# Performance work log

Measured on AMD Instinct MI355X. Metric: run time of the kernel, lower is better.

## Reference

```python
import jax, jax.numpy as jnp
import numpy as np
from jax import lax

T_MAX, BATCH, CLASSES, L_MAX = 512, 32, 1296, 64
NINF = -jnp.inf


def _align_one(logsm, label, C, R):
    """Monotonic max-probability forced alignment for one sample.
    logsm: [T, V] log-probs, label: [L] int, C=x_len (valid frames), R=label_len.
    Returns per-frame pseudo target [T] (0-padded past C)."""
    T, V = logsm.shape
    L = label.shape[0]
    rows = jnp.arange(L)
    cols = jnp.arange(T)
    # pb[i, j] = logsm[j, label[i]], restricted to the monotonic band i <= j <= C-R+i
    pb = logsm[:, label].T  # [L, T]
    band = (cols[None, :] >= rows[:, None]) & (cols[None, :] <= C - R + rows[:, None]) & (rows[:, None] < R)
    pb = jnp.where(band, pb, NINF)

    # Forward DP over time columns: dp[i,j] = max(dp[i-1,j-1], dp[i,j-1]) + pb[i,j]
    # (strict > for the diagonal move, exactly as the original numpy code).
    dp0 = jnp.where(rows == 0, pb[:, 0], NINF)

    def step(dp, pb_col):
        shifted = jnp.concatenate([jnp.full((1,), NINF, dp.dtype), dp[:-1]])
        choice = shifted > dp  # True -> came from (i-1, j-1)
        dp_new = jnp.where(choice, shifted, dp) + pb_col
        return dp_new, choice

    _, choices = lax.scan(step, dp0, pb.T[1:])  # [T-1, L] bool
    choices = jnp.concatenate([jnp.zeros((1, L), bool), choices], axis=0)  # [T, L]

    # Backtrack from (R-1, C-1); columns j >= C emit padding 0.
    def bstep(row, jc):
        j, ch = jc
        active = j < C
        tgt = jnp.where(active, label[row], 0)
        row_new = jnp.where(active, row - ch[row].astype(row.dtype), row)
        return row_new, tgt

    row0 = (R - 1).astype(jnp.int32)
    _, targets = lax.scan(bstep, row0, (jnp.arange(T), choices), reverse=True)
    return targets  # [T]


def _make_targets(logsm, label, x_len, label_len):
    # logsm: [T, B, V] -> targets [T, B]
    return jax.vmap(_align_one, in_axes=(1, 0, 0, 0))(logsm, label, x_len, label_len).T


def setup_inputs() -> dict:
    key = jax.random.key(0)
    k0, k1, k2, k3, k4 = jax.random.split(key, 5)
    pred = jax.random.normal(k0, (T_MAX, BATCH, CLASSES), jnp.float32)
    seq_pred = jax.random.normal(k1, (T_MAX, BATCH, CLASSES), jnp.float32)
    label = jax.random.randint(k2, (BATCH, L_MAX), 0, CLASSES)
    x_len = jax.random.randint(k3, (BATCH,), T_MAX // 2, T_MAX + 1)  # >= L_MAX so band is valid
    label_len = jax.random.randint(k4, (BATCH,), 8, L_MAX + 1)
    return {"pred": pred, "seq_pred": seq_pred, "label": label, "x_len": x_len, "label_len": label_len}


def reference(pred, seq_pred, label, x_len, label_len):
    T, B, V = pred.shape
    logsm_seq = jax.nn.log_softmax(seq_pred, axis=-1)
    target = _make_targets(logsm_seq, label, x_len, label_len)  # [T, B] int
    probs = jnp.exp(logsm_seq)  # softmax(seq_pred)
    conf = jnp.take_along_axis(probs, target[..., None], axis=2)[..., 0]  # [T, B]
    smooth = (1.0 - conf) / (V - 1)
    onehot = jax.nn.one_hot(target, V, dtype=pred.dtype)  # [T, B, V]
    true_dist = jnp.where(onehot > 0, conf[..., None], smooth[..., None])
    mask = (jnp.arange(T)[:, None] < x_len[None, :]).astype(pred.dtype)  # [T, B]
    ce = jnp.sum(-true_dist * jax.nn.log_softmax(pred, axis=-1), axis=-1) * mask
    return jnp.mean(ce)
```

## Files before the change

kernel.cpp:

```cpp
#include <hip/hip_runtime.h>

#define T_MAX 512
#define BATCH 32
#define CLASSES 1296
#define L_MAX 64
#define NROWS (T_MAX * BATCH)
#define NV4 (CLASSES / 4)
#define NINF (-INFINITY)

__device__ __forceinline__ float wave_sum64(float v) {
    v += __int_as_float(__builtin_amdgcn_update_dpp(0, __float_as_int(v), 0x111, 0xF, 0xF, true));
    v += __int_as_float(__builtin_amdgcn_update_dpp(0, __float_as_int(v), 0x112, 0xF, 0xF, true));
    v += __int_as_float(__builtin_amdgcn_update_dpp(0, __float_as_int(v), 0x114, 0xF, 0xF, true));
    v += __int_as_float(__builtin_amdgcn_update_dpp(0, __float_as_int(v), 0x118, 0xF, 0xF, true));
    v += __int_as_float(__builtin_amdgcn_update_dpp(0, __float_as_int(v), 0x142, 0xF, 0xF, true));
    v += __int_as_float(__builtin_amdgcn_update_dpp(0, __float_as_int(v), 0x143, 0xF, 0xF, true));
    return v;
}

__global__ __launch_bounds__(256) void rowstats_kernel(
    const float* __restrict__ pred, const float* __restrict__ seqp,
    const int* __restrict__ label,
    float* __restrict__ lse_pred, float* __restrict__ sum_pred,
    float* __restrict__ lse_seq, float* __restrict__ pb, int* __restrict__ counter)
{
    int wid = blockIdx.x * 4 + (threadIdx.x >> 6);
    int lane = threadIdx.x & 63;
    if (wid == 0 && lane == 0) *counter = 0;
    bool isSeq = wid >= NROWS;
    int r = isSeq ? wid - NROWS : wid;
    const float* x = (isSeq ? seqp : pred) + (size_t)r * CLASSES;
    const float4* x4 = (const float4*)x;

    float4 q0 = x4[lane];
    float4 q1 = x4[lane + 64];
    float4 q2 = x4[lane + 128];
    float4 q3 = x4[lane + 192];
    float4 q4 = x4[lane + 256];
    float4 qt = make_float4(0.f, 0.f, 0.f, 0.f);
    if (lane < 4) qt = x4[320 + lane];
    int lab = 0;
    if (isSeq) lab = label[((r & 31) << 6) + lane];

    float s  = __expf(q0.x) + __expf(q0.y) + __expf(q0.z) + __expf(q0.w)
             + __expf(q1.x) + __expf(q1.y) + __expf(q1.z) + __expf(q1.w)
             + __expf(q2.x) + __expf(q2.y) + __expf(q2.z) + __expf(q2.w)
             + __expf(q3.x) + __expf(q3.y) + __expf(q3.z) + __expf(q3.w)
             + __expf(q4.x) + __expf(q4.y) + __expf(q4.z) + __expf(q4.w);
    float sx = (q0.x + q0.y + q0.z + q0.w) + (q1.x + q1.y + q1.z + q1.w)
             + (q2.x + q2.y + q2.z + q2.w) + (q3.x + q3.y + q3.z + q3.w)
             + (q4.x + q4.y + q4.z + q4.w);
    if (lane < 4) {
        s  += __expf(qt.x) + __expf(qt.y) + __expf(qt.z) + __expf(qt.w);
        sx += qt.x + qt.y + qt.z + qt.w;
    }
    s  = wave_sum64(s);
    sx = wave_sum64(sx);

    if (isSeq) {
        int b = r & 31, t = r >> 5;
        pb[(((size_t)(b << 9) + t) << 6) + lane] = x[lab];
        if (lane == 63) lse_seq[r] = __logf(s);
    } else if (lane == 63) {
        lse_pred[r] = __logf(s);
        sum_pred[r] = sx;
    }
}

__global__ __launch_bounds__(128) void align_kernel(
    const float* __restrict__ pb, const int* __restrict__ x_len,
    const int* __restrict__ label_len, int* __restrict__ tg)
{
    int b = blockIdx.x;
    int tid = threadIdx.x, w = tid >> 6, lane = tid & 63;
    int C = x_len[b], R = label_len[b];
    int limit = C - R;
    __shared__ float buf[2][4096];
    __shared__ unsigned long long ch[T_MAX];
    __shared__ int rows_s[T_MAX];
    const float* pbb = pb + ((size_t)b << 15);
    int P = (C + 63) >> 6;

    if (w == 1) {
        const float4* s4 = (const float4*)pbb;
        float4* d4 = (float4*)buf[0];
        #pragma unroll
        for (int k = 0; k < 16; ++k) d4[(k << 6) + lane] = s4[(k << 6) + lane];
    }
    __syncthreads();

    float dp = NINF;
    const int ninf_i = 0xFF800000;

    for (int p = 0; p < P; ++p) {
        if (w == 1) {
            int ldp = p + 1; if (ldp > 7) ldp = 7;
            const float4* s4 = (const float4*)(pbb + (ldp << 12));
            float4* d4 = (float4*)buf[(p + 1) & 1];
            #pragma unroll
            for (int k = 0; k < 16; ++k) d4[(k << 6) + lane] = s4[(k << 6) + lane];
        } else {
            const float* bc = buf[p & 1];
            int base = p << 6;
            unsigned long long m_local = 0ULL;
            #pragma unroll
            for (int g = 0; g < 4; ++g) {
                float v[16];
                #pragma unroll
                for (int u = 0; u < 16; ++u) v[u] = bc[((g << 4) + u) * 64 + lane];
                #pragma unroll
                for (int u = 0; u < 16; ++u) {
                    int kk = (g << 4) + u;
                    int j = base + kk;
                    if (kk == 0 && g == 0 && p == 0) {
                        dp = (lane == 0) ? v[0] : NINF;
                    } else {
                        bool inband = (lane <= j) && (lane >= j - limit) && (lane < R);
                        float val = inband ? v[u] : NINF;
                        int dpb = __float_as_int(dp);
                        int t1 = __builtin_amdgcn_update_dpp(ninf_i, dpb, 0x111, 0xF, 0xF, false);
                        int t2 = __builtin_amdgcn_update_dpp(ninf_i, dpb, 0x142, 0xF, 0xF, false);
                        float shifted = __int_as_float(((lane & 15) == 0) ? t2 : t1);
                        bool c = shifted > dp;
                        unsigned long long msk = __ballot(c);
                        dp = (c ? shifted : dp) + val;
                        m_local = (lane == kk) ? msk : m_local;
                    }
                }
            }
            ch[base + lane] = m_local;
        }
        __syncthreads();
    }

    if (tid == 0) {
        int row = R - 1;
        int j2 = C - 1;
        while (j2 >= 0) {
            int bs = j2 & ~7;
            unsigned long long m[8];
            #pragma unroll
            for (int k = 0; k < 8; ++k) m[k] = ch[bs + k];
            for (int k = j2 - bs; k >= 0; --k) {
                rows_s[bs + k] = row;
                row -= (int)((m[k] >> row) & 1ULL);
            }
            j2 = bs - 1;
        }
    }
    __syncthreads();
    for (int j = tid; j < T_MAX; j += 128)
        tg[(b << 9) + j] = (j < C) ? rows_s[j] : -1;
}

__global__ __launch_bounds__(256) void ce_kernel(
    const float* __restrict__ pred, const int* __restrict__ label,
    const int* __restrict__ x_len,
    const float* __restrict__ lse_pred, const float* __restrict__ sum_pred,
    const float* __restrict__ lse_seq, const float* __restrict__ pb,
    const int* __restrict__ tg, float* __restrict__ partials,
    int* __restrict__ counter, float* __restrict__ out)
{
    int e = blockIdx.x * 256 + threadIdx.x;
    int t = e >> 5, b = e & 31;
    float ce = 0.f;
    if (t < x_len[b]) {
        int row = tg[(b << 9) + t];
        int tgt = label[(b << 6) + row];
        float lp = lse_pred[e];
        float S = sum_pred[e] - (float)CLASSES * lp;
        float lsp_t = pred[(size_t)e * CLASSES + tgt] - lp;
        float conf = __expf(pb[(((size_t)(b << 9) + t) << 6) + row] - lse_seq[e]);
        float smooth = (1.f - conf) * (1.f / (float)(CLASSES - 1));
        ce = -((conf - smooth) * lsp_t + smooth * S);
    }
    ce = wave_sum64(ce);
    __shared__ float sm[4];
    __shared__ int amLast;
    if ((threadIdx.x & 63) == 63) sm[threadIdx.x >> 6] = ce;
    __syncthreads();
    if (threadIdx.x == 0) {
        float p = sm[0] + sm[1] + sm[2] + sm[3];
        __hip_atomic_store(&partials[blockIdx.x], p, __ATOMIC_RELEASE, __HIP_MEMORY_SCOPE_AGENT);
        amLast = (__hip_atomic_fetch_add(counter, 1, __ATOMIC_ACQ_REL, __HIP_MEMORY_SCOPE_AGENT) == 63);
    }
    __syncthreads();
    if (amLast && threadIdx.x < 64) {
        float v = __hip_atomic_load(&partials[threadIdx.x], __ATOMIC_ACQUIRE, __HIP_MEMORY_SCOPE_AGENT);
        for (int o = 32; o; o >>= 1) v += __shfl_down(v, o, 64);
        if (threadIdx.x == 0) out[0] = v * (1.0f / (float)NROWS);
    }
}

extern "C" void kernel_launch(void* const* d_in, const int* in_sizes, int n_in,
                              void* d_out, int out_size, void* d_ws, size_t ws_size,
                              hipStream_t stream) {
    const float* pred      = (const float*)d_in[0];
    const float* seq_pred  = (const float*)d_in[1];
    const int*   label     = (const int*)d_in[2];
    const int*   x_len     = (const int*)d_in[3];
    const int*   label_len = (const int*)d_in[4];
    float* out = (float*)d_out;

    float* w = (float*)d_ws;
    float* lse_pred = w;
    float* sum_pred = w + NROWS;
    float* lse_seq  = w + 2 * NROWS;
    float* pb       = w + 3 * NROWS;
    int*   tg       = (int*)(w + 3 * NROWS + (size_t)BATCH * T_MAX * 64);
    float* partials = (float*)(tg + NROWS);
    int*   counter  = (int*)(partials + 64);

    rowstats_kernel<<<(2 * NROWS) / 4, 256, 0, stream>>>(pred, seq_pred, label,
                                                         lse_pred, sum_pred, lse_seq, pb, counter);
    align_kernel<<<BATCH, 128, 0, stream>>>(pb, x_len, label_len, tg);
    ce_kernel<<<64, 256, 0, stream>>>(pred, label, x_len,
                                      lse_pred, sum_pred, lse_seq, pb, tg,
                                      partials, counter, out);
}
```

Measured before the change: 243.7 us.

## Restructure alignment DP with transposed choice bits and jump backtrack

The row-stats kernel now has each wave handle both the pred and seq_pred row for the same index, halving the grid and sharing the label load. The alignment DP pre-masks rows beyond the label length during the prefetch copy and skips the band test for blocks that lie entirely inside the band. Choice bits are stored per lane as row-major words, replacing the ballot. The serial backtrack now jumps to the highest set bit per row using clz instead of stepping frame by frame, and the rows are filled in parallel. The aim is to shorten the serial DP and backtrack latency, which depends on the exact tie and boundary semantics staying unchanged.

```diff
diff --git a/kernel.cpp b/kernel.cpp
--- a/kernel.cpp
+++ b/kernel.cpp
@@ -24,46 +24,51 @@
     float* __restrict__ lse_pred, float* __restrict__ sum_pred,
     float* __restrict__ lse_seq, float* __restrict__ pb, int* __restrict__ counter)
 {
-    int wid = blockIdx.x * 4 + (threadIdx.x >> 6);
+    int r = blockIdx.x * 4 + (threadIdx.x >> 6);
     int lane = threadIdx.x & 63;
-    if (wid == 0 && lane == 0) *counter = 0;
-    bool isSeq = wid >= NROWS;
-    int r = isSeq ? wid - NROWS : wid;
-    const float* x = (isSeq ? seqp : pred) + (size_t)r * CLASSES;
-    const float4* x4 = (const float4*)x;
-
-    float4 q0 = x4[lane];
-    float4 q1 = x4[lane + 64];
-    float4 q2 = x4[lane + 128];
-    float4 q3 = x4[lane + 192];
-    float4 q4 = x4[lane + 256];
-    float4 qt = make_float4(0.f, 0.f, 0.f, 0.f);
-    if (lane < 4) qt = x4[320 + lane];
-    int lab = 0;
-    if (isSeq) lab = label[((r & 31) << 6) + lane];
-
-    float s  = __expf(q0.x) + __expf(q0.y) + __expf(q0.z) + __expf(q0.w)
-             + __expf(q1.x) + __expf(q1.y) + __expf(q1.z) + __expf(q1.w)
-             + __expf(q2.x) + __expf(q2.y) + __expf(q2.z) + __expf(q2.w)
-             + __expf(q3.x) + __expf(q3.y) + __expf(q3.z) + __expf(q3.w)
-             + __expf(q4.x) + __expf(q4.y) + __expf(q4.z) + __expf(q4.w);
-    float sx = (q0.x + q0.y + q0.z + q0.w) + (q1.x + q1.y + q1.z + q1.w)
-             + (q2.x + q2.y + q2.z + q2.w) + (q3.x + q3.y + q3.z + q3.w)
-             + (q4.x + q4.y + q4.z + q4.w);
+    if (r == 0 && lane == 0) *counter = 0;
+    const float* xp = pred + (size_t)r * CLASSES;
+    const float* xs = seqp + (size_t)r * CLASSES;
+    const float4* p4 = (const float4*)xp;
+    const float4* s4 = (const float4*)xs;
+
+    float4 a0 = p4[lane],       a1 = p4[lane + 64],  a2 = p4[lane + 128];
+    float4 a3 = p4[lane + 192], a4 = p4[lane + 256];
+    float4 b0 = s4[lane],       b1 = s4[lane + 64],  b2 = s4[lane + 128];
+    float4 b3 = s4[lane + 192], b4 = s4[lane + 256];
+    float4 at = make_float4(0.f, 0.f, 0.f, 0.f);
+    float4 bt = make_float4(0.f, 0.f, 0.f, 0.f);
+    if (lane < 4) { at = p4[320 + lane]; bt = s4[320 + lane]; }
+    int lab = label[((r & 31) << 6) + lane];
+
+    float sp = __expf(a0.x) + __expf(a0.y) + __expf(a0.z) + __expf(a0.w)
+             + __expf(a1.x) + __expf(a1.y) + __expf(a1.z) + __expf(a1.w)
+             + __expf(a2.x) + __expf(a2.y) + __expf(a2.z) + __expf(a2.w)
+             + __expf(a3.x) + __expf(a3.y) + __expf(a3.z) + __expf(a3.w)
+             + __expf(a4.x) + __expf(a4.y) + __expf(a4.z) + __expf(a4.w);
+    float sx = (a0.x + a0.y + a0.z + a0.w) + (a1.x + a1.y + a1.z + a1.w)
+             + (a2.x + a2.y + a2.z + a2.w) + (a3.x + a3.y + a3.z + a3.w)
+             + (a4.x + a4.y + a4.z + a4.w);
+    float ss = __expf(b0.x) + __expf(b0.y) + __expf(b0.z) + __expf(b0.w)
+             + __expf(b1.x) + __expf(b1.y) + __expf(b1.z) + __expf(b1.w)
+             + __expf(b2.x) + __expf(b2.y) + __expf(b2.z) + __expf(b2.w)
+             + __expf(b3.x) + __expf(b3.y) + __expf(b3.z) + __expf(b3.w)
+             + __expf(b4.x) + __expf(b4.y) + __expf(b4.z) + __expf(b4.w);
     if (lane < 4) {
-        s  += __expf(qt.x) + __expf(qt.y) + __expf(qt.z) + __expf(qt.w);
-        sx += qt.x + qt.y + qt.z + qt.w;
-    }
-    s  = wave_sum64(s);
+        sp += __expf(at.x) + __expf(at.y) + __expf(at.z) + __expf(at.w);
+        sx += at.x + at.y + at.z + at.w;
+        ss += __expf(bt.x) + __expf(bt.y) + __expf(bt.z) + __expf(bt.w);
+    }
+    sp = wave_sum64(sp);
     sx = wave_sum64(sx);
-
-    if (isSeq) {
-        int b = r & 31, t = r >> 5;
-        pb[(((size_t)(b << 9) + t) << 6) + lane] = x[lab];
-        if (lane == 63) lse_seq[r] = __logf(s);
-    } else if (lane == 63) {
-        lse_pred[r] = __logf(s);
+    ss = wave_sum64(ss);
+
+    int b = r & 31, t = r >> 5;
+    pb[(((size_t)(b << 9) + t) << 6) + lane] = xs[lab];
+    if (lane == 63) {
+        lse_pred[r] = __logf(sp);
         sum_pred[r] = sx;
+        lse_seq[r]  = __logf(ss);
     }
 }
 
@@ -76,77 +81,106 @@
     int C = x_len[b], R = label_len[b];
     int limit = C - R;
     __shared__ float buf[2][4096];
-    __shared__ unsigned long long ch[T_MAX];
+    __shared__ uint2 chw[8 * 64];
+    __shared__ int a_s[64];
     __shared__ int rows_s[T_MAX];
     const float* pbb = pb + ((size_t)b << 15);
     int P = (C + 63) >> 6;
+
+    int l0 = (lane & 15) << 2;
+    bool mk0 = (l0 + 0) < R, mk1 = (l0 + 1) < R, mk2 = (l0 + 2) < R, mk3 = (l0 + 3) < R;
+    bool isb0 = (lane & 15) == 0;
+    const int ninf_i = 0xFF800000;
 
     if (w == 1) {
         const float4* s4 = (const float4*)pbb;
         float4* d4 = (float4*)buf[0];
         #pragma unroll
-        for (int k = 0; k < 16; ++k) d4[(k << 6) + lane] = s4[(k << 6) + lane];
+        for (int k = 0; k < 16; ++k) {
+            float4 q = s4[(k << 6) + lane];
+            q.x = mk0 ? q.x : NINF;  q.y = mk1 ? q.y : NINF;
+            q.z = mk2 ? q.z : NINF;  q.w = mk3 ? q.w : NINF;
+            d4[(k << 6) + lane] = q;
+        }
     }
     __syncthreads();
 
     float dp = NINF;
-    const int ninf_i = 0xFF800000;
-
     for (int p = 0; p < P; ++p) {
         if (w == 1) {
             int ldp = p + 1; if (ldp > 7) ldp = 7;
             const float4* s4 = (const float4*)(pbb + (ldp << 12));
             float4* d4 = (float4*)buf[(p + 1) & 1];
             #pragma unroll
-            for (int k = 0; k < 16; ++k) d4[(k << 6) + lane] = s4[(k << 6) + lane];
+            for (int k = 0; k < 16; ++k) {
+                float4 q = s4[(k << 6) + lane];
+                q.x = mk0 ? q.x : NINF;  q.y = mk1 ? q.y : NINF;
+                q.z = mk2 ? q.z : NINF;  q.w = mk3 ? q.w : NINF;
+                d4[(k << 6) + lane] = q;
+            }
         } else {
             const float* bc = buf[p & 1];
             int base = p << 6;
-            unsigned long long m_local = 0ULL;
+            unsigned w0 = 0, w1 = 0;
             #pragma unroll
             for (int g = 0; g < 4; ++g) {
                 float v[16];
                 #pragma unroll
                 for (int u = 0; u < 16; ++u) v[u] = bc[((g << 4) + u) * 64 + lane];
+                bool general = (p == 0) || (base + (g << 4) + 15 > limit);
                 #pragma unroll
                 for (int u = 0; u < 16; ++u) {
                     int kk = (g << 4) + u;
                     int j = base + kk;
-                    if (kk == 0 && g == 0 && p == 0) {
-                        dp = (lane == 0) ? v[0] : NINF;
+                    float val;
+                    if (general) {
+                        if (p == 0 && kk == 0) {
+                            dp = (lane == 0) ? v[0] : NINF;
+                            continue;
+                        }
+                        bool ib = (lane <= j) && (lane >= j - limit);
+                        val = ib ? v[u] : NINF;
                     } else {
-                        bool inband = (lane <= j) && (lane >= j - limit) && (lane < R);
-                        float val = inband ? v[u] : NINF;
-                        int dpb = __float_as_int(dp);
-                        int t1 = __builtin_amdgcn_update_dpp(ninf_i, dpb, 0x111, 0xF, 0xF, false);
-                        int t2 = __builtin_amdgcn_update_dpp(ninf_i, dpb, 0x142, 0xF, 0xF, false);
-                        float shifted = __int_as_float(((lane & 15) == 0) ? t2 : t1);
-                        bool c = shifted > dp;
-                        unsigned long long msk = __ballot(c);
-                        dp = (c ? shifted : dp) + val;
-                        m_local = (lane == kk) ? msk : m_local;
+                        val = v[u];
                     }
+                    int dpb = __float_as_int(dp);
+                    int t1 = __builtin_amdgcn_update_dpp(ninf_i, dpb, 0x111, 0xF, 0xF, false);
+                    int t2 = __builtin_amdgcn_update_dpp(ninf_i, dpb, 0x142, 0xF, 0xF, false);
+                    float shifted = __int_as_float(isb0 ? t2 : t1);
+                    bool c = shifted > dp;
+                    unsigned bit01 = c ? 1u : 0u;
+                    if (kk < 32) w0 |= bit01 << kk; else w1 |= bit01 << (kk - 32);
+                    dp = fmaxf(shifted, dp) + val;
                 }
             }
-            ch[base + lane] = m_local;
+            chw[(p << 6) + lane] = make_uint2(w0, w1);
         }
         __syncthreads();
     }
 
     if (tid == 0) {
-        int row = R - 1;
-        int j2 = C - 1;
-        while (j2 >= 0) {
-            int bs = j2 & ~7;
-            unsigned long long m[8];
-            #pragma unroll
-            for (int k = 0; k < 8; ++k) m[k] = ch[bs + k];
-            for (int k = j2 - bs; k >= 0; --k) {
-                rows_s[bs + k] = row;
-                row -= (int)((m[k] >> row) & 1ULL);
+        const unsigned* ch32 = (const unsigned*)chw;
+        int row = R - 1, j = C - 1;
+        while (row > 0 && j >= 0) {
+            unsigned word = ch32[((j >> 6) << 7) + (row << 1) + ((j >> 5) & 1)];
+            unsigned mb = (2u << (j & 31)) - 1;
+            unsigned m = word & mb;
+            if (m) {
+                int hb = 31 - __clz(m);
+                int aj = (j & ~31) | hb;
+                a_s[row] = aj;
+                row--; j = aj - 1;
+            } else {
+                j = (j & ~31) - 1;
             }
-            j2 = bs - 1;
         }
+        for (int i = row; i >= 0; --i) a_s[i] = 0;
+    }
+    __syncthreads();
+    if (tid < R) {
+        int a = a_s[tid];
+        int bi = (tid == R - 1) ? (C - 1) : (a_s[tid + 1] - 1);
+        for (int j = a; j <= bi; ++j) rows_s[j] = tid;
     }
     __syncthreads();
     for (int j = tid; j < T_MAX; j += 128)
@@ -211,8 +245,8 @@
     float* partials = (float*)(tg + NROWS);
     int*   counter  = (int*)(partials + 64);
 
-    rowstats_kernel<<<(2 * NROWS) / 4, 256, 0, stream>>>(pred, seq_pred, label,
-                                                         lse_pred, sum_pred, lse_seq, pb, counter);
+    rowstats_kernel<<<NROWS / 4, 256, 0, stream>>>(pred, seq_pred, label,
+                                                   lse_pred, sum_pred, lse_seq, pb, counter);
     align_kernel<<<BATCH, 128, 0, stream>>>(pb, x_len, label_len, tg);
     ce_kernel<<<64, 256, 0, stream>>>(pred, label, x_len,
                                       lse_pred, sum_pred, lse_seq, pb, tg,
```

New measurement: 222.5 us. -8.7%, faster.
